# Performance work log

Hardware: AMD Instinct MI355X
Metric: run time of the kernel (lower is better)

## Reference

```python
import jax, jax.numpy as jnp
import numpy as np

N_NODES = 100000
N_EDGES = 600000
N_GRAPHS = 128
IN_DIM = 4
HID = 32
HEADS1 = 4
NEG_SLOPE = 0.2


def _segment_softmax(e, seg, n):
    # e: [E, H], softmax over edges sharing the same destination node
    m = jax.ops.segment_max(e, seg, num_segments=n)
    ex = jnp.exp(e - m[seg])
    s = jax.ops.segment_sum(ex, seg, num_segments=n)
    return ex / s[seg]


def _gat_layer(x, src, dst, W, a_src, a_dst, b, heads, ch):
    # PyG GATConv: h = x W (per-head), alpha = softmax_dst(leaky_relu(a_s.h_src + a_d.h_dst))
    n = x.shape[0]
    h = (x @ W).reshape(n, heads, ch)                       # [N, H, C]
    al_s = jnp.einsum('nhc,hc->nh', h, a_src)               # [N, H]
    al_d = jnp.einsum('nhc,hc->nh', h, a_dst)
    e = jax.nn.leaky_relu(al_s[src] + al_d[dst], NEG_SLOPE)  # [E, H]
    alpha = _segment_softmax(e, dst, n)                      # [E, H]
    msg = h[src] * alpha[:, :, None]                         # [E, H, C]
    out = jax.ops.segment_sum(msg, dst, num_segments=n)     # [N, H, C]
    return out.reshape(n, heads * ch) + b


def setup_inputs() -> dict:
    key = jax.random.key(0)
    ks = jax.random.split(key, 16)
    s = 0.1
    return {
        'x': jax.random.normal(ks[0], (N_NODES, IN_DIM), jnp.float32),
        'edge_index': jax.random.randint(ks[1], (2, N_EDGES), 0, N_NODES, jnp.int64),
        'batch': jax.random.randint(ks[2], (N_NODES,), 0, N_GRAPHS, jnp.int64),
        'W1': jax.random.normal(ks[3], (IN_DIM, HEADS1 * HID), jnp.float32) * s,
        'a_s1': jax.random.normal(ks[4], (HEADS1, HID), jnp.float32) * s,
        'a_d1': jax.random.normal(ks[5], (HEADS1, HID), jnp.float32) * s,
        'b1': jnp.zeros((HEADS1 * HID,), jnp.float32),
        'W2': jax.random.normal(ks[6], (HEADS1 * HID, HID), jnp.float32) * s,
        'a_s2': jax.random.normal(ks[7], (1, HID), jnp.float32) * s,
        'a_d2': jax.random.normal(ks[8], (1, HID), jnp.float32) * s,
        'b2': jnp.zeros((HID,), jnp.float32),
        'Wc1': jax.random.normal(ks[9], (HID, 32), jnp.float32) * s,
        'bc1': jnp.zeros((32,), jnp.float32),
        'Wc2': jax.random.normal(ks[10], (32, 1), jnp.float32) * s,
        'bc2': jnp.zeros((1,), jnp.float32),
    }


def reference(x, edge_index, batch, W1, a_s1, a_d1, b1, W2, a_s2, a_d2, b2, Wc1, bc1, Wc2, bc2):
    n = x.shape[0]
    loops = jnp.arange(n, dtype=edge_index.dtype)
    src = jnp.concatenate([edge_index[0], loops])   # add_self_loops=True (PyG default)
    dst = jnp.concatenate([edge_index[1], loops])
    h = jax.nn.elu(_gat_layer(x, src, dst, W1, a_s1, a_d1, b1, HEADS1, HID))
    h = jax.nn.elu(_gat_layer(h, src, dst, W2, a_s2, a_d2, b2, 1, HID))
    # global_mean_pool
    sums = jax.ops.segment_sum(h, batch, num_segments=N_GRAPHS)
    cnt = jax.ops.segment_sum(jnp.ones((n, 1), h.dtype), batch, num_segments=N_GRAPHS)
    g = sums / jnp.maximum(cnt, 1.0)
    z = jax.nn.relu(g @ Wc1 + bc1)
    return jax.nn.sigmoid(z @ Wc2 + bc2)
```

## Files before the change

### kernel.cpp

```cpp
#include <hip/hip_runtime.h>
#include <hip/hip_fp16.h>
#include <float.h>

#define NEG 0.2f
#define NPART 16
#define PAD 32

typedef _Float16 half2v __attribute__((ext_vector_type(2)));

__device__ __forceinline__ float lrelu(float x){ return x > 0.f ? x : NEG * x; }
__device__ __forceinline__ float elu1(float x){ return x > 0.f ? x : (__expf(x) - 1.f); }

__global__ void k_scat(const int* __restrict__ ei, const int* __restrict__ batch,
                       int* __restrict__ cur, int* __restrict__ csr_src,
                       float* __restrict__ gcnt, int N, int E){
  __shared__ float gc[128];
  int tid = threadIdx.x;
  bool doh = blockIdx.x < 256;
  if (doh && tid < 128) gc[tid] = 0.f;
  __syncthreads();
  int idx = blockIdx.x * 256 + tid;
  int gstr = gridDim.x * 256;
  for (int e = idx; e < E; e += gstr){
    int s = ei[e], d = ei[E + e];
    int pos = atomicAdd(cur + d, 1);
    if (pos < PAD) csr_src[(size_t)d * PAD + pos] = s;
  }
  if (doh){
    for (int n = idx; n < N; n += 256 * 256)
      atomicAdd(&gc[batch[n]], 1.f);
    __syncthreads();
    if (tid < 128 && gc[tid] != 0.f) atomicAdd(gcnt + tid, gc[tid]);
  }
}

__global__ void __launch_bounds__(256, 6)
k_layer1(const int* __restrict__ degp, const int* __restrict__ csr_src,
         const float* __restrict__ x, const float* __restrict__ W1,
         const float* __restrict__ as1, const float* __restrict__ ad1,
         const float* __restrict__ b1, const float* __restrict__ W2,
         const float* __restrict__ as2, const float* __restrict__ ad2,
         __half* __restrict__ h2h, float* __restrict__ als2,
         float* __restrict__ ald2, int N){
  __shared__ float PQ[2][16];
  __shared__ __align__(16) float xa[32][20];
  __shared__ __align__(16) _Float16 rowsh[4][128];
  __shared__ float als_s[32], ald_s[32];
  int tid = threadIdx.x;
  const float4* x4 = (const float4*)x;

  int g1 = tid >> 3, l = tid & 7;
  int node1 = blockIdx.x * 32 + g1;
  int nd = node1 < N ? node1 : N - 1;
  int deg = degp[nd];
  size_t r0 = (size_t)nd * PAD;
  int s_pre = csr_src[r0 + l];
  int total = (node1 < N) ? deg + 1 : 0;
  int s0 = (l < deg) ? s_pre : nd;
  float4 xv0 = x4[s0];
  float4 xn = x4[nd];

  if (tid < 32){
    int which = tid >> 4, kh = tid & 15, k = kh >> 2, h = kh & 3;
    const float* a = which ? ad1 : as1;
    float s = 0.f;
    #pragma unroll 8
    for (int c = 0; c < 32; c++) s += W1[k*128 + h*32 + c] * a[h*32 + c];
    PQ[which][kh] = s;
  }
  __syncthreads();

  {
    float P[16], Q[16];
    #pragma unroll
    for (int i = 0; i < 16; i++){ P[i] = PQ[0][i]; Q[i] = PQ[1][i]; }
    float ald0 = xn.x*Q[0] + xn.y*Q[4] + xn.z*Q[8]  + xn.w*Q[12];
    float ald1_ = xn.x*Q[1] + xn.y*Q[5] + xn.z*Q[9]  + xn.w*Q[13];
    float ald2_ = xn.x*Q[2] + xn.y*Q[6] + xn.z*Q[10] + xn.w*Q[14];
    float ald3 = xn.x*Q[3] + xn.y*Q[7] + xn.z*Q[11] + xn.w*Q[15];
    float acc[16];
    #pragma unroll
    for (int i = 0; i < 16; i++) acc[i] = 0.f;
    float ss[4] = {0.f, 0.f, 0.f, 0.f};
    if (l < total){
      float4 xv = xv0;
      float a0 = xv.x*P[0] + xv.y*P[4] + xv.z*P[8]  + xv.w*P[12];
      float a1 = xv.x*P[1] + xv.y*P[5] + xv.z*P[9]  + xv.w*P[13];
      float a2 = xv.x*P[2] + xv.y*P[6] + xv.z*P[10] + xv.w*P[14];
      float a3 = xv.x*P[3] + xv.y*P[7] + xv.z*P[11] + xv.w*P[15];
      float e0 = __expf(lrelu(a0 + ald0));
      float e1 = __expf(lrelu(a1 + ald1_));
      float e2 = __expf(lrelu(a2 + ald2_));
      float e3 = __expf(lrelu(a3 + ald3));
      ss[0] += e0; ss[1] += e1; ss[2] += e2; ss[3] += e3;
      acc[0]  += e0*xv.x; acc[1]  += e0*xv.y; acc[2]  += e0*xv.z; acc[3]  += e0*xv.w;
      acc[4]  += e1*xv.x; acc[5]  += e1*xv.y; acc[6]  += e1*xv.z; acc[7]  += e1*xv.w;
      acc[8]  += e2*xv.x; acc[9]  += e2*xv.y; acc[10] += e2*xv.z; acc[11] += e2*xv.w;
      acc[12] += e3*xv.x; acc[13] += e3*xv.y; acc[14] += e3*xv.z; acc[15] += e3*xv.w;
    }
    for (int t = l + 8; t < total; t += 8){
      int s = (t < deg) ? csr_src[r0 + t] : nd;
      float4 xv = x4[s];
      float a0 = xv.x*P[0] + xv.y*P[4] + xv.z*P[8]  + xv.w*P[12];
      float a1 = xv.x*P[1] + xv.y*P[5] + xv.z*P[9]  + xv.w*P[13];
      float a2 = xv.x*P[2] + xv.y*P[6] + xv.z*P[10] + xv.w*P[14];
      float a3 = xv.x*P[3] + xv.y*P[7] + xv.z*P[11] + xv.w*P[15];
      float e0 = __expf(lrelu(a0 + ald0));
      float e1 = __expf(lrelu(a1 + ald1_));
      float e2 = __expf(lrelu(a2 + ald2_));
      float e3 = __expf(lrelu(a3 + ald3));
      ss[0] += e0; ss[1] += e1; ss[2] += e2; ss[3] += e3;
      acc[0]  += e0*xv.x; acc[1]  += e0*xv.y; acc[2]  += e0*xv.z; acc[3]  += e0*xv.w;
      acc[4]  += e1*xv.x; acc[5]  += e1*xv.y; acc[6]  += e1*xv.z; acc[7]  += e1*xv.w;
      acc[8]  += e2*xv.x; acc[9]  += e2*xv.y; acc[10] += e2*xv.z; acc[11] += e2*xv.w;
      acc[12] += e3*xv.x; acc[13] += e3*xv.y; acc[14] += e3*xv.z; acc[15] += e3*xv.w;
    }
    #pragma unroll
    for (int m = 4; m >= 1; m >>= 1){
      #pragma unroll
      for (int i = 0; i < 16; i++) acc[i] += __shfl_xor(acc[i], m, 8);
      #pragma unroll
      for (int i = 0; i < 4; i++)  ss[i]  += __shfl_xor(ss[i], m, 8);
    }
    if (l == 0){
      float* o = xa[g1];
      *(float4*)(o)      = make_float4(acc[0],  acc[1],  acc[2],  acc[3]);
      *(float4*)(o + 4)  = make_float4(acc[4],  acc[5],  acc[6],  acc[7]);
      *(float4*)(o + 8)  = make_float4(acc[8],  acc[9],  acc[10], acc[11]);
      *(float4*)(o + 12) = make_float4(acc[12], acc[13], acc[14], acc[15]);
      *(float4*)(o + 16) = make_float4(ss[0], ss[1], ss[2], ss[3]);
    }
  }
  __syncthreads();
  __builtin_amdgcn_sched_barrier(0);

  int L = tid & 63, w = tid >> 6;
  int half = L >> 5, c = L & 31;
  half2v w2h[32];
  #pragma unroll
  for (int kk = 0; kk < 32; kk++){
    half2v t;
    t.x = (_Float16)W2[(half*64 + 2*kk)*32 + c];
    t.y = (_Float16)W2[(half*64 + 2*kk + 1)*32 + c];
    w2h[kk] = t;
  }
  float w1a[4], w1b[4];
  #pragma unroll
  for (int k = 0; k < 4; k++){ w1a[k] = W1[k*128 + L]; w1b[k] = W1[k*128 + 64 + L]; }
  float b1a = b1[L], b1b = b1[64 + L];
  float asc = as2[c], adc = ad2[c];
  int ha = L >> 5, hb = 2 + (L >> 5);
  _Float16* rwh = rowsh[w];

  for (int i = 0; i < 8; i++){
    int g = w*8 + i;
    int node = blockIdx.x * 32 + g;
    if (node >= N) continue;
    const float* xg = xa[g];
    float4 xva = *(const float4*)(xg + ha*4);
    float4 xvb = *(const float4*)(xg + hb*4);
    float ssa = xg[16 + ha], ssb = xg[16 + hb];
    float oa = elu1((xva.x*w1a[0] + xva.y*w1a[1] + xva.z*w1a[2] + xva.w*w1a[3]) / ssa + b1a);
    float ob = elu1((xvb.x*w1b[0] + xvb.y*w1b[1] + xvb.z*w1b[2] + xvb.w*w1b[3]) / ssb + b1b);
    rwh[L] = (_Float16)oa; rwh[64 + L] = (_Float16)ob;
    __builtin_amdgcn_wave_barrier();
    float p = 0.f;
    const float4* r4 = (const float4*)(rwh + half*64);
    #pragma unroll
    for (int q = 0; q < 8; q++){
      union { float4 f; half2v h[4]; } u;
      u.f = r4[q];
      #pragma unroll
      for (int j = 0; j < 4; j++)
        p = __builtin_amdgcn_fdot2(u.h[j], w2h[q*4 + j], p, false);
    }
    __builtin_amdgcn_wave_barrier();
    p += __shfl_xor(p, 32, 64);
    if (half == 0){
      h2h[(size_t)node*32 + c] = __float2half(p);
      float ps = p * asc, pd = p * adc;
      #pragma unroll
      for (int m = 16; m >= 1; m >>= 1){
        ps += __shfl_xor(ps, m, 32);
        pd += __shfl_xor(pd, m, 32);
      }
      if (c == 0){ als_s[g] = ps; ald_s[g] = pd; }
    }
  }
  __syncthreads();
  if (tid < 32){
    int node = blockIdx.x * 32 + tid;
    if (node < N){ als2[node] = als_s[tid]; ald2[node] = ald_s[tid]; }
  }
}

__global__ void __launch_bounds__(256)
k_gat2(const int* __restrict__ degp, const int* __restrict__ csr_src,
       const __half* __restrict__ h2h, const float* __restrict__ als2,
       const float* __restrict__ ald2, const float* __restrict__ b2,
       const int* __restrict__ batch, float* __restrict__ gsum_part, int N){
  int tid = threadIdx.x;
  int node = blockIdx.x * 8 + (tid >> 5);
  if (node >= N) return;
  int lane = tid & 31;
  int c2 = lane & 15;
  int sub = lane >> 4;
  int deg = degp[node];
  size_t r0 = (size_t)node * PAD;
  int total = deg + 1;
  float ald = ald2[node];

  float ssum = 0.f;
  float fx0 = 0.f, fy0 = 0.f, fx1 = 0.f, fy1 = 0.f;
  for (int base = 0; base < total; base += 32){
    int t = base + lane;
    int s = (t < deg) ? csr_src[r0 + t] : node;
    float ex = (t < total) ? __expf(lrelu(als2[s] + ald)) : 0.f;
    ssum += ex;
    int lim = min(32, total - base);
    int jj = 0;
    for (; jj + 4 <= lim; jj += 4){
      int ja = jj + sub, jb = jj + 2 + sub;
      float ea = __shfl(ex, ja, 32); int sa = __shfl(s, ja, 32);
      float eb = __shfl(ex, jb, 32); int sb = __shfl(s, jb, 32);
      float2 va = __half22float2(*(const __half2*)(h2h + (size_t)sa*32 + 2*c2));
      float2 vb = __half22float2(*(const __half2*)(h2h + (size_t)sb*32 + 2*c2));
      fx0 += ea*va.x; fy0 += ea*va.y;
      fx1 += eb*vb.x; fy1 += eb*vb.y;
    }
    for (; jj < lim; jj += 2){
      int j2 = jj + sub;
      float ej = (j2 < lim) ? __shfl(ex, j2, 32) : 0.f;
      int   sj = __shfl(s, (j2 < lim) ? j2 : jj, 32);
      float2 v = __half22float2(*(const __half2*)(h2h + (size_t)sj*32 + 2*c2));
      fx0 += ej*v.x; fy0 += ej*v.y;
    }
  }
  float fx = fx0 + fx1, fy = fy0 + fy1;
  fx += __shfl_xor(fx, 16, 32);
  fy += __shfl_xor(fy, 16, 32);
  #pragma unroll
  for (int m = 16; m >= 1; m >>= 1) ssum += __shfl_xor(ssum, m, 32);
  float fc = sub ? fy : fx;
  int ch = 2*c2 + sub;
  float v = elu1(fc / ssum + b2[ch]);
  int b = batch[node];
  atomicAdd(gsum_part + ((blockIdx.x & (NPART-1)) << 12) + b*32 + ch, v);
}

__global__ void k_head(const float* __restrict__ gsum_part, const float* __restrict__ gcnt,
                       const float* __restrict__ Wc1, const float* __restrict__ bc1,
                       const float* __restrict__ Wc2, const float* __restrict__ bc2,
                       float* __restrict__ out){
  int g = blockIdx.x, tid = threadIdx.x;
  __shared__ float gl[32];
  if (tid < 32){
    float s = 0.f;
    #pragma unroll
    for (int p = 0; p < NPART; p++) s += gsum_part[(p << 12) + g*32 + tid];
    float cnt = gcnt[g];
    cnt = cnt > 1.f ? cnt : 1.f;
    gl[tid] = s / cnt;
  }
  __syncthreads();
  if (tid < 32){
    float z = bc1[tid];
    #pragma unroll 8
    for (int c2 = 0; c2 < 32; c2++) z += gl[c2] * Wc1[c2*32 + tid];
    z = z > 0.f ? z : 0.f;
    float r = z * Wc2[tid];
    #pragma unroll
    for (int m = 16; m >= 1; m >>= 1) r += __shfl_xor(r, m, 32);
    if (tid == 0) out[g] = 1.f / (1.f + expf(-(r + bc2[0])));
  }
}

extern "C" void kernel_launch(void* const* d_in, const int* in_sizes, int n_in,
                              void* d_out, int out_size, void* d_ws, size_t ws_size,
                              hipStream_t stream){
  const float* x   = (const float*)d_in[0];
  const int*   ei  = (const int*)d_in[1];
  const int*   bat = (const int*)d_in[2];
  const float* W1  = (const float*)d_in[3];
  const float* as1 = (const float*)d_in[4];
  const float* ad1 = (const float*)d_in[5];
  const float* b1  = (const float*)d_in[6];
  const float* W2  = (const float*)d_in[7];
  const float* as2 = (const float*)d_in[8];
  const float* ad2 = (const float*)d_in[9];
  const float* b2  = (const float*)d_in[10];
  const float* Wc1 = (const float*)d_in[11];
  const float* bc1 = (const float*)d_in[12];
  const float* Wc2 = (const float*)d_in[13];
  const float* bc2 = (const float*)d_in[14];
  float* out = (float*)d_out;

  const int N = in_sizes[2];
  const int E = in_sizes[1] / 2;

  float* ws = (float*)d_ws;
  size_t off = 0;
  int* cur    = (int*)ws;           off += (size_t)N;
  float* gsum_part = ws + off;      off += (size_t)NPART * 4096;
  float* gcnt = ws + off;           off += 128;
  const size_t zero_elems = off;
  __half* h2h = (__half*)(ws + off); off += (size_t)N * 16;
  float* als2 = ws + off;           off += (size_t)N;
  float* ald2 = ws + off;           off += (size_t)N;
  int* csr_src= (int*)(ws + off);   off += (size_t)N * PAD;

  hipMemsetAsync(d_ws, 0, zero_elems * sizeof(float), stream);

  k_scat<<<(E + 255) / 256, 256, 0, stream>>>(ei, bat, cur, csr_src, gcnt, N, E);

  k_layer1<<<(N + 31) / 32, 256, 0, stream>>>(cur, csr_src, x, W1, as1, ad1, b1,
                                              W2, as2, ad2, h2h, als2, ald2, N);

  k_gat2<<<(N + 7) / 8, 256, 0, stream>>>(cur, csr_src, h2h, als2, ald2, b2,
                                          bat, gsum_part, N);

  k_head<<<128, 64, 0, stream>>>(gsum_part, gcnt, Wc1, bc1, Wc2, bc2, out);
}
```

Measured before the change: 194.5 us.

## Compute layer-2 projection with MFMA 16x16x32 f16 instead of per-node fdot2 loop

Replaces the per-wave serial loop, which computed one node's 128->32 projection at a time with fdot2 and shuffles, with a block-wide scheme. All 32 nodes' ELU outputs are first written to shared memory as f16, then four waves each compute a 16x16 tile with MFMA 16x16x32. The attention dot products are then done by 8 threads per node with a shorter shuffle reduction. It also replaces the per-element divide with a precomputed reciprocal. The change adds shared memory and extra block barriers, which could lower occupancy.

```diff
diff --git a/kernel.cpp b/kernel.cpp
--- a/kernel.cpp
+++ b/kernel.cpp
@@ -6,7 +6,8 @@
 #define NPART 16
 #define PAD 32
 
-typedef _Float16 half2v __attribute__((ext_vector_type(2)));
+typedef _Float16 half8 __attribute__((ext_vector_type(8)));
+typedef float f32x4 __attribute__((ext_vector_type(4)));
 
 __device__ __forceinline__ float lrelu(float x){ return x > 0.f ? x : NEG * x; }
 __device__ __forceinline__ float elu1(float x){ return x > 0.f ? x : (__expf(x) - 1.f); }
@@ -44,7 +45,8 @@
          float* __restrict__ ald2, int N){
   __shared__ float PQ[2][16];
   __shared__ __align__(16) float xa[32][20];
-  __shared__ __align__(16) _Float16 rowsh[4][128];
+  __shared__ __align__(16) _Float16 out1sh[32][136];
+  __shared__ __align__(16) float h2sh[32][36];
   __shared__ float als_s[32], ald_s[32];
   int tid = threadIdx.x;
   const float4* x4 = (const float4*)x;
@@ -132,60 +134,71 @@
     }
   }
   __syncthreads();
+  if (tid < 128) xa[tid >> 2][16 + (tid & 3)] = 1.f / xa[tid >> 2][16 + (tid & 3)];
   __builtin_amdgcn_sched_barrier(0);
 
-  int L = tid & 63, w = tid >> 6;
-  int half = L >> 5, c = L & 31;
-  half2v w2h[32];
+  int wv = tid >> 6, lane = tid & 63;
+  int wm = wv >> 1, wn = wv & 1;
+  int lrow = lane & 15, lk8 = lane >> 4;
+  half8 bf[4];
   #pragma unroll
-  for (int kk = 0; kk < 32; kk++){
-    half2v t;
-    t.x = (_Float16)W2[(half*64 + 2*kk)*32 + c];
-    t.y = (_Float16)W2[(half*64 + 2*kk + 1)*32 + c];
-    w2h[kk] = t;
-  }
-  float w1a[4], w1b[4];
+  for (int t = 0; t < 4; t++){
+    #pragma unroll
+    for (int j = 0; j < 8; j++)
+      bf[t][j] = (_Float16)W2[(t*32 + lk8*8 + j)*32 + wn*16 + lrow];
+  }
+  int c128 = ((wv & 1) << 6) | lane;
+  int gbase = (wv >> 1) << 4;
+  int hh = c128 >> 5;
+  float w1c0 = W1[c128], w1c1 = W1[128 + c128];
+  float w1c2 = W1[256 + c128], w1c3 = W1[384 + c128];
+  float b1c = b1[c128];
+  __syncthreads();
+
   #pragma unroll
-  for (int k = 0; k < 4; k++){ w1a[k] = W1[k*128 + L]; w1b[k] = W1[k*128 + 64 + L]; }
-  float b1a = b1[L], b1b = b1[64 + L];
-  float asc = as2[c], adc = ad2[c];
-  int ha = L >> 5, hb = 2 + (L >> 5);
-  _Float16* rwh = rowsh[w];
-
-  for (int i = 0; i < 8; i++){
-    int g = w*8 + i;
+  for (int i = 0; i < 16; i++){
+    int g = gbase + i;
+    const float* xg = xa[g];
+    float4 xv = *(const float4*)(xg + hh*4);
+    float rs = xg[16 + hh];
+    float o = elu1((xv.x*w1c0 + xv.y*w1c1 + xv.z*w1c2 + xv.w*w1c3) * rs + b1c);
+    out1sh[g][c128] = (_Float16)o;
+  }
+  __syncthreads();
+
+  {
+    f32x4 acc2 = {0.f, 0.f, 0.f, 0.f};
+    #pragma unroll
+    for (int t = 0; t < 4; t++){
+      half8 af = *(const half8*)(&out1sh[wm*16 + lrow][t*32 + lk8*8]);
+      acc2 = __builtin_amdgcn_mfma_f32_16x16x32_f16(af, bf[t], acc2, 0, 0, 0);
+    }
+    #pragma unroll
+    for (int i = 0; i < 4; i++)
+      h2sh[wm*16 + lk8*4 + i][wn*16 + lrow] = acc2[i];
+  }
+  __syncthreads();
+
+  {
+    int g = tid >> 3, q = tid & 7;
     int node = blockIdx.x * 32 + g;
-    if (node >= N) continue;
-    const float* xg = xa[g];
-    float4 xva = *(const float4*)(xg + ha*4);
-    float4 xvb = *(const float4*)(xg + hb*4);
-    float ssa = xg[16 + ha], ssb = xg[16 + hb];
-    float oa = elu1((xva.x*w1a[0] + xva.y*w1a[1] + xva.z*w1a[2] + xva.w*w1a[3]) / ssa + b1a);
-    float ob = elu1((xvb.x*w1b[0] + xvb.y*w1b[1] + xvb.z*w1b[2] + xvb.w*w1b[3]) / ssb + b1b);
-    rwh[L] = (_Float16)oa; rwh[64 + L] = (_Float16)ob;
-    __builtin_amdgcn_wave_barrier();
-    float p = 0.f;
-    const float4* r4 = (const float4*)(rwh + half*64);
-    #pragma unroll
-    for (int q = 0; q < 8; q++){
-      union { float4 f; half2v h[4]; } u;
-      u.f = r4[q];
-      #pragma unroll
-      for (int j = 0; j < 4; j++)
-        p = __builtin_amdgcn_fdot2(u.h[j], w2h[q*4 + j], p, false);
-    }
-    __builtin_amdgcn_wave_barrier();
-    p += __shfl_xor(p, 32, 64);
-    if (half == 0){
-      h2h[(size_t)node*32 + c] = __float2half(p);
-      float ps = p * asc, pd = p * adc;
-      #pragma unroll
-      for (int m = 16; m >= 1; m >>= 1){
-        ps += __shfl_xor(ps, m, 32);
-        pd += __shfl_xor(pd, m, 32);
-      }
-      if (c == 0){ als_s[g] = ps; ald_s[g] = pd; }
-    }
+    float4 hv = *(const float4*)(&h2sh[g][q*4]);
+    if (node < N){
+      __half2 pa = __floats2half2_rn(hv.x, hv.y);
+      __half2 pb = __floats2half2_rn(hv.z, hv.w);
+      __half2* dst = (__half2*)(h2h + (size_t)node*32 + q*4);
+      dst[0] = pa; dst[1] = pb;
+    }
+    float4 sa = *(const float4*)(as2 + q*4);
+    float4 da = *(const float4*)(ad2 + q*4);
+    float ps = hv.x*sa.x + hv.y*sa.y + hv.z*sa.z + hv.w*sa.w;
+    float pd = hv.x*da.x + hv.y*da.y + hv.z*da.z + hv.w*da.w;
+    #pragma unroll
+    for (int m = 4; m >= 1; m >>= 1){
+      ps += __shfl_xor(ps, m, 8);
+      pd += __shfl_xor(pd, m, 8);
+    }
+    if (q == 0){ als_s[g] = ps; ald_s[g] = pd; }
   }
   __syncthreads();
   if (tid < 32){
```

Result: faster. 173.8 us (-10.7%).
